# Optimization experiments

Measured on AMD Instinct MI355X. Metric: run time of the kernel, lower is better.

Reference implementation:

```python
import jax, jax.numpy as jnp
import numpy as np
from jax import lax

EPS = 1e-5

@jax.custom_vjp
def binarize(x):
    return jnp.sign(x)

def _bin_fwd(x):
    return jnp.sign(x), x

def _bin_bwd(x, g):
    # straight-through estimator: pass grad where |x| <= 1
    return (g * (jnp.abs(x) <= 1.0).astype(g.dtype),)

binarize.defvjp(_bin_fwd, _bin_bwd)


def bconv(x, w, stride=1, pad=0):
    # BinarizeConv2d: sign-binarize both activations and weights, dense conv
    return lax.conv_general_dilated(
        binarize(x), binarize(w),
        window_strides=(stride, stride),
        padding=[(pad, pad), (pad, pad)],
        dimension_numbers=('NCHW', 'OIHW', 'NCHW'))


def bn(x, gamma, beta):
    # training-mode batch norm (grad enabled in torch forward): batch stats over (N,H,W)
    mean = x.mean(axis=(0, 2, 3), keepdims=True)
    var = ((x - mean) ** 2).mean(axis=(0, 2, 3), keepdims=True)
    return gamma * (x - mean) * lax.rsqrt(var + EPS) + beta


def hardtanh(x):
    return jnp.clip(x, -1.0, 1.0)


def setup_inputs() -> dict:
    key = jax.random.key(0)
    ks = jax.random.split(key, 4)
    N, Cin, H, W = 64, 256, 56, 56
    P = 64  # planes; expansion*planes == Cin -> identity shortcut
    return {
        'x':  jax.random.normal(ks[0], (N, Cin, H, W), dtype=jnp.float32),
        'w1': jax.random.normal(ks[1], (P, Cin, 1, 1), dtype=jnp.float32),
        'w2': jax.random.normal(ks[2], (P, P, 3, 3), dtype=jnp.float32),
        'w3': jax.random.normal(ks[3], (Cin, P, 1, 1), dtype=jnp.float32),
        'g1': jnp.ones((1, P, 1, 1), jnp.float32),
        'b1': jnp.zeros((1, P, 1, 1), jnp.float32),
        'g2': jnp.ones((1, P, 1, 1), jnp.float32),
        'b2': jnp.zeros((1, P, 1, 1), jnp.float32),
        'g3': jnp.ones((1, Cin, 1, 1), jnp.float32),
        'b3': jnp.zeros((1, Cin, 1, 1), jnp.float32),
    }


def reference(x, w1, w2, w3, g1, b1, g2, b2, g3, b3):
    out = hardtanh(bn(bconv(x, w1), g1, b1))                 # 1x1 binconv + BN + hardtanh
    out = hardtanh(bn(bconv(out, w2, stride=1, pad=1), g2, b2))  # 3x3 binconv + BN + hardtanh
    out = bn(bconv(out, w3), g3, b3)                          # 1x1 binconv + BN
    out = out + x                                             # identity shortcut
    return hardtanh(out)
```

## Files before the change

### kernel.cpp

```cpp
#include <hip/hip_runtime.h>
#include <stdint.h>
#include <math.h>

typedef unsigned long long u64;
typedef long long ll;

#define H_    56
#define W_    56
#define HW_   3136
#define N_    64
#define C_    256
#define P_    64
#define NPIX_ 200704
#define BN_EPS 1e-5

__global__ __launch_bounds__(256) void pack_weights_k(
    const float* __restrict__ w1, const float* __restrict__ w2,
    const float* __restrict__ w3,
    u64* __restrict__ ws1, u64* __restrict__ wn1,
    u64* __restrict__ ws2, u64* __restrict__ wn2, int* __restrict__ b2,
    u64* __restrict__ ws3, u64* __restrict__ wn3, int* __restrict__ b3) {
  int t = blockIdx.x * 256 + threadIdx.x;
  if (t < 64) {
    int co = t;
    for (int ch = 0; ch < 4; ++ch) {
      u64 s = 0, n = 0;
      for (int j = 0; j < 64; ++j) {
        float v = w1[co * 256 + ch * 64 + j];
        s |= ((u64)(v < 0.f)) << j;
        n |= ((u64)(v != 0.f)) << j;
      }
      ws1[co * 4 + ch] = s; wn1[co * 4 + ch] = n;
    }
  } else if (t < 64 + 576) {
    int idx = t - 64, co = idx / 9, tap = idx % 9;
    u64 s = 0, n = 0;
    for (int ci = 0; ci < 64; ++ci) {
      float v = w2[(co * 64 + ci) * 9 + tap];
      s |= ((u64)(v < 0.f)) << ci;
      n |= ((u64)(v != 0.f)) << ci;
    }
    ws2[idx] = s; wn2[idx] = n; b2[idx] = __popcll(n);
  } else if (t < 64 + 576 + 256) {
    int co = t - 640;
    u64 s = 0, n = 0;
    for (int ci = 0; ci < 64; ++ci) {
      float v = w3[co * 64 + ci];
      s |= ((u64)(v < 0.f)) << ci;
      n |= ((u64)(v != 0.f)) << ci;
    }
    ws3[co] = s; wn3[co] = n; b3[co] = __popcll(n);
  }
}

__global__ __launch_bounds__(256) void pack_x_k(
    const float* __restrict__ x, u64* __restrict__ xs, u64* __restrict__ xn) {
  int p = blockIdx.x * 256 + threadIdx.x;
  int n = p / HW_, hw = p % HW_;
  const float* xb = x + (size_t)n * C_ * HW_ + hw;
  for (int ch = 0; ch < 4; ++ch) {
    u64 s = 0, nb = 0;
    for (int j = 0; j < 64; ++j) {
      float v = xb[(size_t)(ch * 64 + j) * HW_];
      s |= ((u64)(v < 0.f)) << j;
      nb |= ((u64)(v != 0.f)) << j;
    }
    xs[(size_t)p * 4 + ch] = s;
    xn[(size_t)p * 4 + ch] = nb;
  }
}

__global__ __launch_bounds__(256) void conv1_k(
    const u64* __restrict__ xs, const u64* __restrict__ xn,
    const u64* __restrict__ ws1, const u64* __restrict__ wn1,
    short* __restrict__ y, u64* __restrict__ gsum, u64* __restrict__ gsq) {
  __shared__ u64 lws[256], lwn[256];
  __shared__ int reds[4][64], redq[4][64];
  int tx = threadIdx.x, ty = threadIdx.y, lidx = ty * 64 + tx;
  lws[lidx] = ws1[lidx]; lwn[lidx] = wn1[lidx];
  __syncthreads();
  int s_acc = 0, q_acc = 0;
  int base = blockIdx.x * 256;
  for (int i = 0; i < 64; ++i) {
    int p = base + i * 4 + ty;
    u64 s0 = xs[(size_t)p*4+0], s1 = xs[(size_t)p*4+1],
        s2 = xs[(size_t)p*4+2], s3 = xs[(size_t)p*4+3];
    u64 n0 = xn[(size_t)p*4+0], n1 = xn[(size_t)p*4+1],
        n2 = xn[(size_t)p*4+2], n3 = xn[(size_t)p*4+3];
    int acc = 0;
    {
      u64 v, a;
      v = n0 & lwn[tx*4+0]; a = ~(s0 ^ lws[tx*4+0]) & v; acc += 2*__popcll(a) - __popcll(v);
      v = n1 & lwn[tx*4+1]; a = ~(s1 ^ lws[tx*4+1]) & v; acc += 2*__popcll(a) - __popcll(v);
      v = n2 & lwn[tx*4+2]; a = ~(s2 ^ lws[tx*4+2]) & v; acc += 2*__popcll(a) - __popcll(v);
      v = n3 & lwn[tx*4+3]; a = ~(s3 ^ lws[tx*4+3]) & v; acc += 2*__popcll(a) - __popcll(v);
    }
    y[(size_t)p * 64 + tx] = (short)acc;
    s_acc += acc; q_acc += acc * acc;
  }
  reds[ty][tx] = s_acc; redq[ty][tx] = q_acc;
  __syncthreads();
  if (ty == 0) {
    int s = reds[0][tx] + reds[1][tx] + reds[2][tx] + reds[3][tx];
    int q = redq[0][tx] + redq[1][tx] + redq[2][tx] + redq[3][tx];
    atomicAdd(&gsum[tx], (u64)(ll)s);
    atomicAdd(&gsq[tx],  (u64)(ll)q);
  }
}

__global__ void finalize_bn_k(const u64* __restrict__ gsum,
                              const u64* __restrict__ gsq,
                              const float* __restrict__ gamma,
                              const float* __restrict__ beta,
                              double* __restrict__ dsc, double* __restrict__ dsh,
                              int ch) {
  int c = blockIdx.x * blockDim.x + threadIdx.x;
  if (c < ch) {
    double S = (double)(ll)gsum[c], Q = (double)(ll)gsq[c];
    double mean = S / (double)NPIX_;
    double var  = Q / (double)NPIX_ - mean * mean;
    double inv  = 1.0 / sqrt(var + BN_EPS);
    double sc   = (double)gamma[c] * inv;
    dsc[c] = sc;
    dsh[c] = (double)beta[c] - mean * sc;
  }
}

__global__ __launch_bounds__(256) void binarize_pack_k(
    const short* __restrict__ y, const double* __restrict__ dsc,
    const double* __restrict__ dsh, u64* __restrict__ pout) {
  int lane = threadIdx.x & 63, wid = threadIdx.x >> 6;
  double sc = dsc[lane], sh = dsh[lane];
  int base = blockIdx.x * 256;
  for (int i = 0; i < 64; ++i) {
    int p = base + i * 4 + wid;
    int v = (int)y[(size_t)p * 64 + lane];
    u64 m = __ballot(sc * (double)v + sh < 0.0);
    if (lane == 0) pout[p] = m;
  }
}

__global__ __launch_bounds__(256) void conv2_k(
    const u64* __restrict__ p1,
    const u64* __restrict__ ws2, const u64* __restrict__ wn2,
    const int* __restrict__ b2,
    short* __restrict__ y, u64* __restrict__ gsum, u64* __restrict__ gsq) {
  __shared__ u64 lws[576], lwn[576];
  __shared__ int lb[576];
  __shared__ int reds[4][64], redq[4][64];
  int tx = threadIdx.x, ty = threadIdx.y, lidx = ty * 64 + tx;
  for (int j = lidx; j < 576; j += 256) { lws[j] = ws2[j]; lwn[j] = wn2[j]; lb[j] = b2[j]; }
  __syncthreads();
  int s_acc = 0, q_acc = 0;
  int base = blockIdx.x * 256;
  for (int i = 0; i < 64; ++i) {
    int p = base + i * 4 + ty;
    int n = p / HW_, hw = p % HW_, h = hw / W_, w = hw % W_;
    u64 tv[9]; bool ok[9];
    #pragma unroll
    for (int dh = -1; dh <= 1; ++dh)
      #pragma unroll
      for (int dw = -1; dw <= 1; ++dw) {
        int k = (dh + 1) * 3 + (dw + 1);
        int h2 = h + dh, w2c = w + dw;
        bool v = (h2 >= 0) & (h2 < H_) & (w2c >= 0) & (w2c < W_);
        ok[k] = v;
        tv[k] = v ? p1[n * HW_ + h2 * W_ + w2c] : 0ULL;
      }
    int acc = 0;
    #pragma unroll
    for (int k = 0; k < 9; ++k) {
      int wi = tx * 9 + k;
      u64 a = ~(tv[k] ^ lws[wi]) & lwn[wi];
      int d = 2 * __popcll(a) - lb[wi];
      acc += ok[k] ? d : 0;
    }
    y[(size_t)p * 64 + tx] = (short)acc;
    s_acc += acc; q_acc += acc * acc;
  }
  reds[ty][tx] = s_acc; redq[ty][tx] = q_acc;
  __syncthreads();
  if (ty == 0) {
    int s = reds[0][tx] + reds[1][tx] + reds[2][tx] + reds[3][tx];
    int q = redq[0][tx] + redq[1][tx] + redq[2][tx] + redq[3][tx];
    atomicAdd(&gsum[tx], (u64)(ll)s);
    atomicAdd(&gsq[tx],  (u64)(ll)q);
  }
}

__global__ __launch_bounds__(256) void conv3_stats_k(
    const u64* __restrict__ p2,
    const u64* __restrict__ ws3, const u64* __restrict__ wn3,
    const int* __restrict__ b3,
    u64* __restrict__ gsum, u64* __restrict__ gsq) {
  int t = threadIdx.x;
  u64 s3 = ws3[t], n3 = wn3[t];
  int bb = b3[t];
  int s = 0, q = 0;
  int base = blockIdx.x * 256;
  for (int i = 0; i < 256; ++i) {
    u64 m = p2[base + i];
    int yv = 2 * __popcll(~(m ^ s3) & n3) - bb;
    s += yv; q += yv * yv;
  }
  atomicAdd(&gsum[t], (u64)(ll)s);
  atomicAdd(&gsq[t],  (u64)(ll)q);
}

__global__ __launch_bounds__(256) void final_k(
    const float* __restrict__ x, const u64* __restrict__ p2,
    const u64* __restrict__ ws3, const u64* __restrict__ wn3,
    const int* __restrict__ b3,
    const double* __restrict__ dsc3, const double* __restrict__ dsh3,
    float* __restrict__ out) {
  size_t i4 = (size_t)blockIdx.x * 256 + threadIdx.x;
  size_t idx = i4 * 4;
  int co = (int)((idx / HW_) % C_);
  int nn = (int)(idx / ((size_t)HW_ * C_));
  int hw = (int)(idx % HW_);
  int pb = nn * HW_ + hw;
  u64 s3 = ws3[co], n3 = wn3[co];
  int bb = b3[co];
  float sc = (float)dsc3[co], sh = (float)dsh3[co];
  float4 xv = *(const float4*)(x + idx);
  float4 ov;
  {
    int y0 = 2 * __popcll(~(p2[pb + 0] ^ s3) & n3) - bb;
    int y1 = 2 * __popcll(~(p2[pb + 1] ^ s3) & n3) - bb;
    int y2 = 2 * __popcll(~(p2[pb + 2] ^ s3) & n3) - bb;
    int y3 = 2 * __popcll(~(p2[pb + 3] ^ s3) & n3) - bb;
    ov.x = fminf(fmaxf(sc * (float)y0 + sh + xv.x, -1.f), 1.f);
    ov.y = fminf(fmaxf(sc * (float)y1 + sh + xv.y, -1.f), 1.f);
    ov.z = fminf(fmaxf(sc * (float)y2 + sh + xv.z, -1.f), 1.f);
    ov.w = fminf(fmaxf(sc * (float)y3 + sh + xv.w, -1.f), 1.f);
  }
  *(float4*)(out + idx) = ov;
}

extern "C" void kernel_launch(void* const* d_in, const int* in_sizes, int n_in,
                              void* d_out, int out_size, void* d_ws, size_t ws_size,
                              hipStream_t stream) {
  const float* x  = (const float*)d_in[0];
  const float* w1 = (const float*)d_in[1];
  const float* w2 = (const float*)d_in[2];
  const float* w3 = (const float*)d_in[3];
  const float* g1 = (const float*)d_in[4];
  const float* b1 = (const float*)d_in[5];
  const float* g2 = (const float*)d_in[6];
  const float* b2 = (const float*)d_in[7];
  const float* g3 = (const float*)d_in[8];
  const float* b3 = (const float*)d_in[9];
  float* out = (float*)d_out;

  char* base = (char*)d_ws;
  size_t off = 0;
  auto alloc = [&](size_t bytes) -> char* {
    char* p = base + off;
    off = (off + bytes + 255) & ~(size_t)255;
    return p;
  };
  u64* xs   = (u64*)alloc((size_t)NPIX_ * 4 * 8);
  u64* xn   = (u64*)alloc((size_t)NPIX_ * 4 * 8);
  u64* p1   = (u64*)alloc((size_t)NPIX_ * 8);
  u64* p2   = (u64*)alloc((size_t)NPIX_ * 8);
  short* yb = (short*)alloc((size_t)NPIX_ * 64 * 2);
  u64* ws1  = (u64*)alloc(256 * 8);
  u64* wn1  = (u64*)alloc(256 * 8);
  u64* ws2  = (u64*)alloc(576 * 8);
  u64* wn2  = (u64*)alloc(576 * 8);
  int* bb2  = (int*)alloc(576 * 4);
  u64* ws3  = (u64*)alloc(256 * 8);
  u64* wn3  = (u64*)alloc(256 * 8);
  int* bb3  = (int*)alloc(256 * 4);
  char* stats = alloc(768 * 8);
  u64* sum1 = (u64*)stats;          u64* sq1 = sum1 + 64;
  u64* sum2 = sq1 + 64;             u64* sq2 = sum2 + 64;
  u64* sum3 = sq2 + 64;             u64* sq3 = sum3 + 256;
  double* dsc1 = (double*)alloc(64 * 8);
  double* dsh1 = (double*)alloc(64 * 8);
  double* dsc2 = (double*)alloc(64 * 8);
  double* dsh2 = (double*)alloc(64 * 8);
  double* dsc3 = (double*)alloc(256 * 8);
  double* dsh3 = (double*)alloc(256 * 8);
  (void)ws_size; (void)n_in; (void)in_sizes; (void)out_size;

  hipMemsetAsync(stats, 0, 768 * 8, stream);

  pack_weights_k<<<4, 256, 0, stream>>>(w1, w2, w3, ws1, wn1, ws2, wn2, bb2,
                                        ws3, wn3, bb3);
  pack_x_k<<<784, 256, 0, stream>>>(x, xs, xn);

  dim3 blk(64, 4);
  conv1_k<<<784, blk, 0, stream>>>(xs, xn, ws1, wn1, yb, sum1, sq1);
  finalize_bn_k<<<1, 64, 0, stream>>>(sum1, sq1, g1, b1, dsc1, dsh1, 64);
  binarize_pack_k<<<784, 256, 0, stream>>>(yb, dsc1, dsh1, p1);

  conv2_k<<<784, blk, 0, stream>>>(p1, ws2, wn2, bb2, yb, sum2, sq2);
  finalize_bn_k<<<1, 64, 0, stream>>>(sum2, sq2, g2, b2, dsc2, dsh2, 64);
  binarize_pack_k<<<784, 256, 0, stream>>>(yb, dsc2, dsh2, p2);

  conv3_stats_k<<<784, 256, 0, stream>>>(p2, ws3, wn3, bb3, sum3, sq3);
  finalize_bn_k<<<1, 256, 0, stream>>>(sum3, sq3, g3, b3, dsc3, dsh3, 256);

  final_k<<<50176, 256, 0, stream>>>(x, p2, ws3, wn3, bb3, dsc3, dsh3, out);
}
```

Measured before the change: 639.8 us.

## Fuse x packing into conv1, switch to channel-major outputs, fold BN finalize into consumers

Merges the activation packing and the first 1x1 binary conv into one kernel, so the packed xs/xn buffers are no longer written and reread. Both convs now assign one pixel per thread looping over output channels and store channel-major shorts, which makes the stores coalesced. Per-channel stats are reduced with wave shuffles and shared atomics. The separate BN finalize kernels are removed, with scale and shift recomputed inside binpack and final, and conv3_stats gets fewer, longer blocks. In exchange, each thread's serial loop over 64 channels limits parallelism within a block, and the BN parameters are recomputed redundantly in every block.

After: 613.9 us. -4.0%, faster.

```diff
diff --git a/kernel.cpp b/kernel.cpp
--- a/kernel.cpp
+++ b/kernel.cpp
@@ -53,138 +53,135 @@
   }
 }
 
-__global__ __launch_bounds__(256) void pack_x_k(
-    const float* __restrict__ x, u64* __restrict__ xs, u64* __restrict__ xn) {
-  int p = blockIdx.x * 256 + threadIdx.x;
+__global__ __launch_bounds__(256) void fused1_k(
+    const float* __restrict__ x,
+    const u64* __restrict__ ws1, const u64* __restrict__ wn1,
+    short* __restrict__ y1, u64* __restrict__ gsum, u64* __restrict__ gsq) {
+  __shared__ u64 lws[256], lwn[256];
+  __shared__ int ssum[64], ssq[64];
+  int tid = threadIdx.x;
+  lws[tid] = ws1[tid]; lwn[tid] = wn1[tid];
+  if (tid < 64) { ssum[tid] = 0; ssq[tid] = 0; }
+  __syncthreads();
+
+  int p = blockIdx.x * 256 + tid;
   int n = p / HW_, hw = p % HW_;
-  const float* xb = x + (size_t)n * C_ * HW_ + hw;
+  const float* xb = x + (size_t)n * (C_ * HW_) + hw;
+  u64 s[4], nb[4];
+  #pragma unroll
   for (int ch = 0; ch < 4; ++ch) {
-    u64 s = 0, nb = 0;
+    u64 sv = 0, nv = 0;
+    #pragma unroll
     for (int j = 0; j < 64; ++j) {
-      float v = xb[(size_t)(ch * 64 + j) * HW_];
-      s |= ((u64)(v < 0.f)) << j;
-      nb |= ((u64)(v != 0.f)) << j;
-    }
-    xs[(size_t)p * 4 + ch] = s;
-    xn[(size_t)p * 4 + ch] = nb;
-  }
-}
-
-__global__ __launch_bounds__(256) void conv1_k(
-    const u64* __restrict__ xs, const u64* __restrict__ xn,
-    const u64* __restrict__ ws1, const u64* __restrict__ wn1,
-    short* __restrict__ y, u64* __restrict__ gsum, u64* __restrict__ gsq) {
-  __shared__ u64 lws[256], lwn[256];
-  __shared__ int reds[4][64], redq[4][64];
-  int tx = threadIdx.x, ty = threadIdx.y, lidx = ty * 64 + tx;
-  lws[lidx] = ws1[lidx]; lwn[lidx] = wn1[lidx];
-  __syncthreads();
-  int s_acc = 0, q_acc = 0;
-  int base = blockIdx.x * 256;
-  for (int i = 0; i < 64; ++i) {
-    int p = base + i * 4 + ty;
-    u64 s0 = xs[(size_t)p*4+0], s1 = xs[(size_t)p*4+1],
-        s2 = xs[(size_t)p*4+2], s3 = xs[(size_t)p*4+3];
-    u64 n0 = xn[(size_t)p*4+0], n1 = xn[(size_t)p*4+1],
-        n2 = xn[(size_t)p*4+2], n3 = xn[(size_t)p*4+3];
+      float v = xb[(size_t)((ch * 64 + j) * HW_)];
+      sv |= ((u64)(v < 0.f)) << j;
+      nv |= ((u64)(v != 0.f)) << j;
+    }
+    s[ch] = sv; nb[ch] = nv;
+  }
+
+  int lane = tid & 63;
+  for (int co = 0; co < 64; ++co) {
     int acc = 0;
-    {
-      u64 v, a;
-      v = n0 & lwn[tx*4+0]; a = ~(s0 ^ lws[tx*4+0]) & v; acc += 2*__popcll(a) - __popcll(v);
-      v = n1 & lwn[tx*4+1]; a = ~(s1 ^ lws[tx*4+1]) & v; acc += 2*__popcll(a) - __popcll(v);
-      v = n2 & lwn[tx*4+2]; a = ~(s2 ^ lws[tx*4+2]) & v; acc += 2*__popcll(a) - __popcll(v);
-      v = n3 & lwn[tx*4+3]; a = ~(s3 ^ lws[tx*4+3]) & v; acc += 2*__popcll(a) - __popcll(v);
-    }
-    y[(size_t)p * 64 + tx] = (short)acc;
-    s_acc += acc; q_acc += acc * acc;
-  }
-  reds[ty][tx] = s_acc; redq[ty][tx] = q_acc;
-  __syncthreads();
-  if (ty == 0) {
-    int s = reds[0][tx] + reds[1][tx] + reds[2][tx] + reds[3][tx];
-    int q = redq[0][tx] + redq[1][tx] + redq[2][tx] + redq[3][tx];
-    atomicAdd(&gsum[tx], (u64)(ll)s);
-    atomicAdd(&gsq[tx],  (u64)(ll)q);
-  }
-}
-
-__global__ void finalize_bn_k(const u64* __restrict__ gsum,
-                              const u64* __restrict__ gsq,
-                              const float* __restrict__ gamma,
-                              const float* __restrict__ beta,
-                              double* __restrict__ dsc, double* __restrict__ dsh,
-                              int ch) {
-  int c = blockIdx.x * blockDim.x + threadIdx.x;
-  if (c < ch) {
-    double S = (double)(ll)gsum[c], Q = (double)(ll)gsq[c];
+    #pragma unroll
+    for (int ch = 0; ch < 4; ++ch) {
+      u64 v = nb[ch] & lwn[co * 4 + ch];
+      u64 a = ~(s[ch] ^ lws[co * 4 + ch]) & v;
+      acc += 2 * __popcll(a) - __popcll(v);
+    }
+    y1[(size_t)co * NPIX_ + p] = (short)acc;
+    int rs = acc, rq = acc * acc;
+    #pragma unroll
+    for (int m = 32; m; m >>= 1) {
+      rs += __shfl_xor(rs, m, 64);
+      rq += __shfl_xor(rq, m, 64);
+    }
+    if (lane == 0) { atomicAdd(&ssum[co], rs); atomicAdd(&ssq[co], rq); }
+  }
+  __syncthreads();
+  if (tid < 64) {
+    atomicAdd(&gsum[tid], (u64)(ll)ssum[tid]);
+    atomicAdd(&gsq[tid],  (u64)(ll)ssq[tid]);
+  }
+}
+
+__global__ __launch_bounds__(256) void binpack_k(
+    const short* __restrict__ y,
+    const u64* __restrict__ gsum, const u64* __restrict__ gsq,
+    const float* __restrict__ gamma, const float* __restrict__ beta,
+    u64* __restrict__ pout) {
+  __shared__ double tsc[64], tsh[64];
+  int tid = threadIdx.x;
+  if (tid < 64) {
+    double S = (double)(ll)gsum[tid], Q = (double)(ll)gsq[tid];
     double mean = S / (double)NPIX_;
     double var  = Q / (double)NPIX_ - mean * mean;
     double inv  = 1.0 / sqrt(var + BN_EPS);
-    double sc   = (double)gamma[c] * inv;
-    dsc[c] = sc;
-    dsh[c] = (double)beta[c] - mean * sc;
-  }
-}
-
-__global__ __launch_bounds__(256) void binarize_pack_k(
-    const short* __restrict__ y, const double* __restrict__ dsc,
-    const double* __restrict__ dsh, u64* __restrict__ pout) {
-  int lane = threadIdx.x & 63, wid = threadIdx.x >> 6;
-  double sc = dsc[lane], sh = dsh[lane];
-  int base = blockIdx.x * 256;
-  for (int i = 0; i < 64; ++i) {
-    int p = base + i * 4 + wid;
-    int v = (int)y[(size_t)p * 64 + lane];
-    u64 m = __ballot(sc * (double)v + sh < 0.0);
-    if (lane == 0) pout[p] = m;
-  }
+    double sc   = (double)gamma[tid] * inv;
+    tsc[tid] = sc;
+    tsh[tid] = (double)beta[tid] - mean * sc;
+  }
+  __syncthreads();
+  int p = blockIdx.x * 256 + tid;
+  u64 m = 0;
+  #pragma unroll 8
+  for (int co = 0; co < 64; ++co) {
+    int v = (int)y[(size_t)co * NPIX_ + p];
+    m |= ((u64)(tsc[co] * (double)v + tsh[co] < 0.0)) << co;
+  }
+  pout[p] = m;
 }
 
 __global__ __launch_bounds__(256) void conv2_k(
     const u64* __restrict__ p1,
     const u64* __restrict__ ws2, const u64* __restrict__ wn2,
     const int* __restrict__ b2,
-    short* __restrict__ y, u64* __restrict__ gsum, u64* __restrict__ gsq) {
+    short* __restrict__ y2, u64* __restrict__ gsum, u64* __restrict__ gsq) {
   __shared__ u64 lws[576], lwn[576];
   __shared__ int lb[576];
-  __shared__ int reds[4][64], redq[4][64];
-  int tx = threadIdx.x, ty = threadIdx.y, lidx = ty * 64 + tx;
-  for (int j = lidx; j < 576; j += 256) { lws[j] = ws2[j]; lwn[j] = wn2[j]; lb[j] = b2[j]; }
-  __syncthreads();
-  int s_acc = 0, q_acc = 0;
-  int base = blockIdx.x * 256;
-  for (int i = 0; i < 64; ++i) {
-    int p = base + i * 4 + ty;
-    int n = p / HW_, hw = p % HW_, h = hw / W_, w = hw % W_;
-    u64 tv[9]; bool ok[9];
-    #pragma unroll
-    for (int dh = -1; dh <= 1; ++dh)
-      #pragma unroll
-      for (int dw = -1; dw <= 1; ++dw) {
-        int k = (dh + 1) * 3 + (dw + 1);
-        int h2 = h + dh, w2c = w + dw;
-        bool v = (h2 >= 0) & (h2 < H_) & (w2c >= 0) & (w2c < W_);
-        ok[k] = v;
-        tv[k] = v ? p1[n * HW_ + h2 * W_ + w2c] : 0ULL;
-      }
+  __shared__ int ssum[64], ssq[64];
+  int tid = threadIdx.x;
+  for (int j = tid; j < 576; j += 256) { lws[j] = ws2[j]; lwn[j] = wn2[j]; lb[j] = b2[j]; }
+  if (tid < 64) { ssum[tid] = 0; ssq[tid] = 0; }
+  __syncthreads();
+
+  int p = blockIdx.x * 256 + tid;
+  int n = p / HW_, hw = p % HW_, h = hw / W_, w = hw % W_;
+  u64 tv[9]; bool ok[9];
+  #pragma unroll
+  for (int dh = -1; dh <= 1; ++dh)
+    #pragma unroll
+    for (int dw = -1; dw <= 1; ++dw) {
+      int k = (dh + 1) * 3 + (dw + 1);
+      int h2 = h + dh, w2c = w + dw;
+      bool v = (h2 >= 0) & (h2 < H_) & (w2c >= 0) & (w2c < W_);
+      ok[k] = v;
+      tv[k] = v ? p1[n * HW_ + h2 * W_ + w2c] : 0ULL;
+    }
+
+  int lane = tid & 63;
+  for (int co = 0; co < 64; ++co) {
     int acc = 0;
     #pragma unroll
     for (int k = 0; k < 9; ++k) {
-      int wi = tx * 9 + k;
+      int wi = co * 9 + k;
       u64 a = ~(tv[k] ^ lws[wi]) & lwn[wi];
       int d = 2 * __popcll(a) - lb[wi];
       acc += ok[k] ? d : 0;
     }
-    y[(size_t)p * 64 + tx] = (short)acc;
-    s_acc += acc; q_acc += acc * acc;
-  }
-  reds[ty][tx] = s_acc; redq[ty][tx] = q_acc;
-  __syncthreads();
-  if (ty == 0) {
-    int s = reds[0][tx] + reds[1][tx] + reds[2][tx] + reds[3][tx];
-    int q = redq[0][tx] + redq[1][tx] + redq[2][tx] + redq[3][tx];
-    atomicAdd(&gsum[tx], (u64)(ll)s);
-    atomicAdd(&gsq[tx],  (u64)(ll)q);
+    y2[(size_t)co * NPIX_ + p] = (short)acc;
+    int rs = acc, rq = acc * acc;
+    #pragma unroll
+    for (int m = 32; m; m >>= 1) {
+      rs += __shfl_xor(rs, m, 64);
+      rq += __shfl_xor(rq, m, 64);
+    }
+    if (lane == 0) { atomicAdd(&ssum[co], rs); atomicAdd(&ssq[co], rq); }
+  }
+  __syncthreads();
+  if (tid < 64) {
+    atomicAdd(&gsum[tid], (u64)(ll)ssum[tid]);
+    atomicAdd(&gsq[tid],  (u64)(ll)ssq[tid]);
   }
 }
 
@@ -197,8 +194,9 @@
   u64 s3 = ws3[t], n3 = wn3[t];
   int bb = b3[t];
   int s = 0, q = 0;
-  int base = blockIdx.x * 256;
-  for (int i = 0; i < 256; ++i) {
+  int base = blockIdx.x * 512;
+  #pragma unroll 4
+  for (int i = 0; i < 512; ++i) {
     u64 m = p2[base + i];
     int yv = 2 * __popcll(~(m ^ s3) & n3) - bb;
     s += yv; q += yv * yv;
@@ -211,29 +209,44 @@
     const float* __restrict__ x, const u64* __restrict__ p2,
     const u64* __restrict__ ws3, const u64* __restrict__ wn3,
     const int* __restrict__ b3,
-    const double* __restrict__ dsc3, const double* __restrict__ dsh3,
+    const u64* __restrict__ gsum, const u64* __restrict__ gsq,
+    const float* __restrict__ gamma, const float* __restrict__ beta,
     float* __restrict__ out) {
-  size_t i4 = (size_t)blockIdx.x * 256 + threadIdx.x;
-  size_t idx = i4 * 4;
-  int co = (int)((idx / HW_) % C_);
-  int nn = (int)(idx / ((size_t)HW_ * C_));
+  __shared__ float fsc[2], fsh[2];
+  size_t base = (size_t)blockIdx.x * 1024;
+  size_t r0 = base / HW_;
+  if (threadIdx.x < 2) {
+    int c = (int)((r0 + threadIdx.x) % C_);
+    double S = (double)(ll)gsum[c], Q = (double)(ll)gsq[c];
+    double mean = S / (double)NPIX_;
+    double var  = Q / (double)NPIX_ - mean * mean;
+    double inv  = 1.0 / sqrt(var + BN_EPS);
+    double sc   = (double)gamma[c] * inv;
+    fsc[threadIdx.x] = (float)sc;
+    fsh[threadIdx.x] = (float)((double)beta[c] - mean * sc);
+  }
+  __syncthreads();
+
+  size_t idx = base + (size_t)threadIdx.x * 4;
+  size_t lin = idx / HW_;
+  int rr = (int)(lin - r0);
+  int co = (int)(lin % C_);
+  int nn = (int)(lin / C_);
   int hw = (int)(idx % HW_);
   int pb = nn * HW_ + hw;
   u64 s3 = ws3[co], n3 = wn3[co];
   int bb = b3[co];
-  float sc = (float)dsc3[co], sh = (float)dsh3[co];
+  float sc = fsc[rr], sh = fsh[rr];
   float4 xv = *(const float4*)(x + idx);
   float4 ov;
-  {
-    int y0 = 2 * __popcll(~(p2[pb + 0] ^ s3) & n3) - bb;
-    int y1 = 2 * __popcll(~(p2[pb + 1] ^ s3) & n3) - bb;
-    int y2 = 2 * __popcll(~(p2[pb + 2] ^ s3) & n3) - bb;
-    int y3 = 2 * __popcll(~(p2[pb + 3] ^ s3) & n3) - bb;
-    ov.x = fminf(fmaxf(sc * (float)y0 + sh + xv.x, -1.f), 1.f);
-    ov.y = fminf(fmaxf(sc * (float)y1 + sh + xv.y, -1.f), 1.f);
-    ov.z = fminf(fmaxf(sc * (float)y2 + sh + xv.z, -1.f), 1.f);
-    ov.w = fminf(fmaxf(sc * (float)y3 + sh + xv.w, -1.f), 1.f);
-  }
+  int y0 = 2 * __popcll(~(p2[pb + 0] ^ s3) & n3) - bb;
+  int y1 = 2 * __popcll(~(p2[pb + 1] ^ s3) & n3) - bb;
+  int y2 = 2 * __popcll(~(p2[pb + 2] ^ s3) & n3) - bb;
+  int y3 = 2 * __popcll(~(p2[pb + 3] ^ s3) & n3) - bb;
+  ov.x = fminf(fmaxf(sc * (float)y0 + sh + xv.x, -1.f), 1.f);
+  ov.y = fminf(fmaxf(sc * (float)y1 + sh + xv.y, -1.f), 1.f);
+  ov.z = fminf(fmaxf(sc * (float)y2 + sh + xv.z, -1.f), 1.f);
+  ov.w = fminf(fmaxf(sc * (float)y3 + sh + xv.w, -1.f), 1.f);
   *(float4*)(out + idx) = ov;
 }
 
@@ -259,11 +272,9 @@
     off = (off + bytes + 255) & ~(size_t)255;
     return p;
   };
-  u64* xs   = (u64*)alloc((size_t)NPIX_ * 4 * 8);
-  u64* xn   = (u64*)alloc((size_t)NPIX_ * 4 * 8);
+  short* y1b = (short*)alloc((size_t)NPIX_ * 64 * 2);
   u64* p1   = (u64*)alloc((size_t)NPIX_ * 8);
   u64* p2   = (u64*)alloc((size_t)NPIX_ * 8);
-  short* yb = (short*)alloc((size_t)NPIX_ * 64 * 2);
   u64* ws1  = (u64*)alloc(256 * 8);
   u64* wn1  = (u64*)alloc(256 * 8);
   u64* ws2  = (u64*)alloc(576 * 8);
@@ -276,31 +287,21 @@
   u64* sum1 = (u64*)stats;          u64* sq1 = sum1 + 64;
   u64* sum2 = sq1 + 64;             u64* sq2 = sum2 + 64;
   u64* sum3 = sq2 + 64;             u64* sq3 = sum3 + 256;
-  double* dsc1 = (double*)alloc(64 * 8);
-  double* dsh1 = (double*)alloc(64 * 8);
-  double* dsc2 = (double*)alloc(64 * 8);
-  double* dsh2 = (double*)alloc(64 * 8);
-  double* dsc3 = (double*)alloc(256 * 8);
-  double* dsh3 = (double*)alloc(256 * 8);
   (void)ws_size; (void)n_in; (void)in_sizes; (void)out_size;
 
   hipMemsetAsync(stats, 0, 768 * 8, stream);
 
   pack_weights_k<<<4, 256, 0, stream>>>(w1, w2, w3, ws1, wn1, ws2, wn2, bb2,
                                         ws3, wn3, bb3);
-  pack_x_k<<<784, 256, 0, stream>>>(x, xs, xn);
-
-  dim3 blk(64, 4);
-  conv1_k<<<784, blk, 0, stream>>>(xs, xn, ws1, wn1, yb, sum1, sq1);
-  finalize_bn_k<<<1, 64, 0, stream>>>(sum1, sq1, g1, b1, dsc1, dsh1, 64);
-  binarize_pack_k<<<784, 256, 0, stream>>>(yb, dsc1, dsh1, p1);
-
-  conv2_k<<<784, blk, 0, stream>>>(p1, ws2, wn2, bb2, yb, sum2, sq2);
-  finalize_bn_k<<<1, 64, 0, stream>>>(sum2, sq2, g2, b2, dsc2, dsh2, 64);
-  binarize_pack_k<<<784, 256, 0, stream>>>(yb, dsc2, dsh2, p2);
-
-  conv3_stats_k<<<784, 256, 0, stream>>>(p2, ws3, wn3, bb3, sum3, sq3);
-  finalize_bn_k<<<1, 256, 0, stream>>>(sum3, sq3, g3, b3, dsc3, dsh3, 256);
-
-  final_k<<<50176, 256, 0, stream>>>(x, p2, ws3, wn3, bb3, dsc3, dsh3, out);
-}
+
+  fused1_k<<<784, 256, 0, stream>>>(x, ws1, wn1, y1b, sum1, sq1);
+  binpack_k<<<784, 256, 0, stream>>>(y1b, sum1, sq1, g1, b1, p1);
+
+  conv2_k<<<784, 256, 0, stream>>>(p1, ws2, wn2, bb2, y1b, sum2, sq2);
+  binpack_k<<<784, 256, 0, stream>>>(y1b, sum2, sq2, g2, b2, p2);
+
+  conv3_stats_k<<<392, 256, 0, stream>>>(p2, ws3, wn3, bb3, sum3, sq3);
+
+  final_k<<<50176, 256, 0, stream>>>(x, p2, ws3, wn3, bb3, sum3, sq3, g3, b3,
+                                     out);
+}
```
